# Performance work log

Measured on AMD Instinct MI355X. Metric: run time of the kernel, lower is better.

## Reference

```python
import jax, jax.numpy as jnp
import numpy as np

N_QUBITS = 4
N_LAYERS = 2
DIM = 2 ** N_QUBITS


def _cnot_perm(c, t, n=N_QUBITS):
    # statevector index bit for wire w is at shift (n-1-w)
    idx = np.arange(2 ** n)
    cbit = (idx >> (n - 1 - c)) & 1
    return np.where(cbit == 1, idx ^ (1 << (n - 1 - t)), idx)


def _apply_cnot(state, c, t):
    # state: [B, 2,2,2,2]; CNOT is a basis permutation (its own inverse)
    B = state.shape[0]
    flat = state.reshape(B, DIM)
    return flat[:, _cnot_perm(c, t)].reshape(state.shape)


def _apply_1q(state, U, wire):
    # shared 2x2 gate U on given wire
    st = jnp.moveaxis(state, wire + 1, -1)
    st = jnp.einsum('b...a,ca->b...c', st, U)
    return jnp.moveaxis(st, -1, wire + 1)


def _quantum_circuit(z, weights):
    """AngleEmbedding(RY) + StronglyEntanglingLayers, PauliZ expvals.
    z: [B, n_qubits] angles, weights: [L, n_qubits, 3]. Returns [B, n_qubits]."""
    n = N_QUBITS
    B = z.shape[0]
    state = jnp.zeros((B, DIM), jnp.complex64).at[:, 0].set(1.0)
    state = state.reshape((B,) + (2,) * n)
    # Angle embedding: batched RY(z_w) on each wire
    for w in range(n):
        a = z[:, w] * 0.5
        c, s = jnp.cos(a), jnp.sin(a)
        U = jnp.stack([jnp.stack([c, -s], -1), jnp.stack([s, c], -1)], -2)  # [B,2,2]
        st = jnp.moveaxis(state, w + 1, -1)
        st = jnp.einsum('b...a,bca->b...c', st, U.astype(jnp.complex64))
        state = jnp.moveaxis(st, -1, w + 1)
    # StronglyEntanglingLayers
    for l in range(N_LAYERS):
        for w in range(n):
            phi, theta, omega = weights[l, w, 0], weights[l, w, 1], weights[l, w, 2]
            ct, st_ = jnp.cos(theta * 0.5), jnp.sin(theta * 0.5)
            e_m = jnp.exp(-0.5j * (phi + omega).astype(jnp.complex64))
            e_d = jnp.exp(0.5j * (phi - omega).astype(jnp.complex64))
            U = jnp.stack([
                jnp.stack([e_m * ct, -e_d * st_]),
                jnp.stack([jnp.conj(e_d) * st_, jnp.conj(e_m) * ct]),
            ])  # Rot(phi,theta,omega) = RZ(omega) RY(theta) RZ(phi)
            state = _apply_1q(state, U, w)
        r = (l % (n - 1)) + 1
        for w in range(n):
            state = _apply_cnot(state, w, (w + r) % n)
    probs = state.real ** 2 + state.imag ** 2  # [B,2,2,2,2]
    evs = []
    rest = tuple(range(1, n))
    for w in range(n):
        p = jnp.moveaxis(probs, w + 1, 1)
        evs.append(jnp.sum(p[:, 0], axis=rest) - jnp.sum(p[:, 1], axis=rest))
    return jnp.stack(evs, -1)


def setup_inputs() -> dict:
    key = jax.random.key(0)
    ks = jax.random.split(key, 6)
    B, C, H, W = 16, 256, 128, 128
    return {
        'x': jax.random.normal(ks[0], (B, C, H, W), jnp.float32),
        'enc_w': jax.random.normal(ks[1], (N_QUBITS, C), jnp.float32) / np.sqrt(C),
        'enc_b': jax.random.normal(ks[2], (N_QUBITS,), jnp.float32) * 0.01,
        'qweights': jax.random.uniform(ks[3], (N_LAYERS, N_QUBITS, 3), jnp.float32, 0.0, 2.0 * np.pi),
        'proj_w': jax.random.normal(ks[4], (C, N_QUBITS), jnp.float32) / np.sqrt(N_QUBITS),
        'proj_b': jax.random.normal(ks[5], (C,), jnp.float32) * 0.01,
    }


def reference(x, enc_w, enc_b, qweights, proj_w, proj_b):
    pooled = jnp.mean(x, axis=(2, 3))                      # AdaptiveAvgPool2d(1)+Flatten -> [B,C]
    z = jnp.tanh(pooled @ enc_w.T + enc_b)                 # [B, n_qubits]
    refined = _quantum_circuit(z, qweights)                # [B, n_qubits]
    gates = jax.nn.sigmoid(refined @ proj_w.T + proj_b)    # [B, C]
    return x + x * gates[:, :, None, None]
```

## Files before the change

### kernel.cpp

```cpp
#include <hip/hip_runtime.h>
#include <math.h>

#define NQ 4
#define NL 2
#define DIM 16
#define BATCH 16
#define CH 256
#define HW 16384

typedef float floatx4 __attribute__((ext_vector_type(4)));

__global__ void pool_kernel(const float* __restrict__ x, float* __restrict__ pooled) {
    const int bc = blockIdx.x;
    const floatx4* x4 = (const floatx4*)(x + (size_t)bc * HW);
    const int tid = threadIdx.x;
    float s = 0.f;
#pragma unroll
    for (int k = 0; k < 16; ++k) {
        floatx4 v = x4[tid + k * 256];
        s += v.x + v.y + v.z + v.w;
    }
#pragma unroll
    for (int off = 32; off > 0; off >>= 1) s += __shfl_down(s, off, 64);
    __shared__ float partial[4];
    if ((tid & 63) == 0) partial[tid >> 6] = s;
    __syncthreads();
    if (tid == 0)
        pooled[bc] = (partial[0] + partial[1] + partial[2] + partial[3]) * (1.0f / HW);
}

__global__ void gate_kernel16(const float* __restrict__ pooled,
                              const float* __restrict__ enc_w,
                              const float* __restrict__ enc_b,
                              const float* __restrict__ qw,
                              const float* __restrict__ proj_w,
                              const float* __restrict__ proj_b,
                              float* __restrict__ gates1p) {
    const int b = blockIdx.x;
    const int tid = threadIdx.x;

    __shared__ float sz[NQ];
    __shared__ float sevs[NQ];

    {
        const int q = tid >> 6, lane = tid & 63;
        const float* prow = pooled + b * CH;
        float acc = 0.f;
#pragma unroll
        for (int j = 0; j < 4; ++j) {
            const int c = lane * 4 + j;
            acc += prow[c] * enc_w[q * CH + c];
        }
#pragma unroll
        for (int off = 32; off > 0; off >>= 1) acc += __shfl_down(acc, off, 64);
        if (lane == 0) sz[q] = tanhf(acc + enc_b[q]);
    }
    __syncthreads();

    if (tid == 0) {
        float re[DIM], im[DIM];
#pragma unroll
        for (int i = 0; i < DIM; ++i) { re[i] = 0.f; im[i] = 0.f; }
        re[0] = 1.f;

        for (int w = 0; w < NQ; ++w) {
            const float a = sz[w] * 0.5f;
            const float cc = cosf(a), ss = sinf(a);
            const int m = 1 << (3 - w);
#pragma unroll
            for (int i = 0; i < DIM; ++i) {
                if (i & m) continue;
                const int j = i | m;
                const float r0 = cc * re[i] - ss * re[j];
                const float i0 = cc * im[i] - ss * im[j];
                const float r1 = ss * re[i] + cc * re[j];
                const float i1 = ss * im[i] + cc * im[j];
                re[i] = r0; im[i] = i0; re[j] = r1; im[j] = i1;
            }
        }
        for (int l = 0; l < NL; ++l) {
            for (int w = 0; w < NQ; ++w) {
                const float phi = qw[(l * NQ + w) * 3 + 0];
                const float th  = qw[(l * NQ + w) * 3 + 1];
                const float om  = qw[(l * NQ + w) * 3 + 2];
                const float ct = cosf(0.5f * th), st = sinf(0.5f * th);
                const float am = -0.5f * (phi + om);
                const float ad =  0.5f * (phi - om);
                const float emr = cosf(am), emi = sinf(am);
                const float edr = cosf(ad), edi = sinf(ad);
                const float u00r =  emr * ct, u00i =  emi * ct;
                const float u01r = -edr * st, u01i = -edi * st;
                const float u10r =  edr * st, u10i = -edi * st;
                const float u11r =  emr * ct, u11i = -emi * ct;
                const int m = 1 << (3 - w);
#pragma unroll
                for (int i = 0; i < DIM; ++i) {
                    if (i & m) continue;
                    const int j = i | m;
                    const float ar = re[i], ai = im[i], br = re[j], bi = im[j];
                    re[i] = u00r * ar - u00i * ai + u01r * br - u01i * bi;
                    im[i] = u00r * ai + u00i * ar + u01r * bi + u01i * br;
                    re[j] = u10r * ar - u10i * ai + u11r * br - u11i * bi;
                    im[j] = u10r * ai + u10i * ar + u11r * bi + u11i * br;
                }
            }
            const int r = (l % (NQ - 1)) + 1;
            for (int w = 0; w < NQ; ++w) {
                const int t = (w + r) % NQ;
                const int cm = 1 << (3 - w);
                const int tm = 1 << (3 - t);
#pragma unroll
                for (int i = 0; i < DIM; ++i) {
                    if ((i & cm) && !(i & tm)) {
                        const int j = i | tm;
                        float tr = re[i]; re[i] = re[j]; re[j] = tr;
                        float ti = im[i]; im[i] = im[j]; im[j] = ti;
                    }
                }
            }
        }
        float p[DIM];
#pragma unroll
        for (int i = 0; i < DIM; ++i) p[i] = re[i] * re[i] + im[i] * im[i];
        for (int w = 0; w < NQ; ++w) {
            const int m = 1 << (3 - w);
            float ev = 0.f;
#pragma unroll
            for (int i = 0; i < DIM; ++i) ev += (i & m) ? -p[i] : p[i];
            sevs[w] = ev;
        }
    }
    __syncthreads();

    {
        const int c = tid;
        const float acc = sevs[0] * proj_w[c * NQ + 0] + sevs[1] * proj_w[c * NQ + 1] +
                          sevs[2] * proj_w[c * NQ + 2] + sevs[3] * proj_w[c * NQ + 3] +
                          proj_b[c];
        gates1p[b * CH + c] = 1.f + 1.f / (1.f + expf(-acc));
    }
}

__global__ void scale_kernel(const float* __restrict__ x,
                             const float* __restrict__ gates1p,
                             float* __restrict__ out) {
    const int slice = 4095 - blockIdx.x;
    const int tid = threadIdx.x;
    const floatx4* x4 = (const floatx4*)(x + (size_t)slice * HW);
    floatx4* o4 = (floatx4*)(out + (size_t)slice * HW);
    const float g = gates1p[slice];
    floatx4 v[16];
#pragma unroll
    for (int k = 0; k < 16; ++k) v[k] = x4[tid + k * 256];
#pragma unroll
    for (int k = 0; k < 16; ++k) {
        v[k] *= g;
        __builtin_nontemporal_store(v[k], &o4[tid + k * 256]);
    }
}

extern "C" void kernel_launch(void* const* d_in, const int* in_sizes, int n_in,
                              void* d_out, int out_size, void* d_ws, size_t ws_size,
                              hipStream_t stream) {
    const float* x      = (const float*)d_in[0];
    const float* enc_w  = (const float*)d_in[1];
    const float* enc_b  = (const float*)d_in[2];
    const float* qw     = (const float*)d_in[3];
    const float* proj_w = (const float*)d_in[4];
    const float* proj_b = (const float*)d_in[5];
    float* out = (float*)d_out;

    float* pooled  = (float*)d_ws;
    float* gates1p = pooled + BATCH * CH;

    pool_kernel<<<BATCH * CH, 256, 0, stream>>>(x, pooled);
    gate_kernel16<<<BATCH, 256, 0, stream>>>(pooled, enc_w, enc_b, qw,
                                             proj_w, proj_b, gates1p);
    scale_kernel<<<BATCH * CH, 256, 0, stream>>>(x, gates1p, out);
}
```

Before: 144.9 us.

## Process batch in four chunks so scale pass rereads x from cache

```diff
diff --git a/kernel.cpp b/kernel.cpp
--- a/kernel.cpp
+++ b/kernel.cpp
@@ -7,11 +7,15 @@
 #define BATCH 16
 #define CH 256
 #define HW 16384
+#define CHUNK_B 4
+#define NCHUNK (BATCH / CHUNK_B)
+#define SLICES_PER_CHUNK (CHUNK_B * CH)
 
 typedef float floatx4 __attribute__((ext_vector_type(4)));
 
-__global__ void pool_kernel(const float* __restrict__ x, float* __restrict__ pooled) {
-    const int bc = blockIdx.x;
+__global__ void pool_kernel(const float* __restrict__ x, float* __restrict__ pooled,
+                            int base_bc) {
+    const int bc = base_bc + blockIdx.x;
     const floatx4* x4 = (const floatx4*)(x + (size_t)bc * HW);
     const int tid = threadIdx.x;
     float s = 0.f;
@@ -35,8 +39,9 @@
                               const float* __restrict__ qw,
                               const float* __restrict__ proj_w,
                               const float* __restrict__ proj_b,
-                              float* __restrict__ gates1p) {
-    const int b = blockIdx.x;
+                              float* __restrict__ gates1p,
+                              int base_b) {
+    const int b = base_b + blockIdx.x;
     const int tid = threadIdx.x;
 
     __shared__ float sz[NQ];
@@ -143,8 +148,9 @@
 
 __global__ void scale_kernel(const float* __restrict__ x,
                              const float* __restrict__ gates1p,
-                             float* __restrict__ out) {
-    const int slice = 4095 - blockIdx.x;
+                             float* __restrict__ out,
+                             int base_bc) {
+    const int slice = base_bc + blockIdx.x;
     const int tid = threadIdx.x;
     const floatx4* x4 = (const floatx4*)(x + (size_t)slice * HW);
     floatx4* o4 = (floatx4*)(out + (size_t)slice * HW);
@@ -173,8 +179,12 @@
     float* pooled  = (float*)d_ws;
     float* gates1p = pooled + BATCH * CH;
 
-    pool_kernel<<<BATCH * CH, 256, 0, stream>>>(x, pooled);
-    gate_kernel16<<<BATCH, 256, 0, stream>>>(pooled, enc_w, enc_b, qw,
-                                             proj_w, proj_b, gates1p);
-    scale_kernel<<<BATCH * CH, 256, 0, stream>>>(x, gates1p, out);
+    for (int k = 0; k < NCHUNK; ++k) {
+        const int base_bc = k * SLICES_PER_CHUNK;
+        const int base_b  = k * CHUNK_B;
+        pool_kernel<<<SLICES_PER_CHUNK, 256, 0, stream>>>(x, pooled, base_bc);
+        gate_kernel16<<<CHUNK_B, 256, 0, stream>>>(pooled, enc_w, enc_b, qw,
+                                                   proj_w, proj_b, gates1p, base_b);
+        scale_kernel<<<SLICES_PER_CHUNK, 256, 0, stream>>>(x, gates1p, out, base_bc);
+    }
 }
```

Result: slower. 229.8 us (+58.6%).

## Fuse gate computation into scale kernel, recomputing circuit per channel block

Applied to the files above, without the earlier changes.

```diff
diff --git a/kernel.cpp b/kernel.cpp
--- a/kernel.cpp
+++ b/kernel.cpp
@@ -29,18 +29,31 @@
         pooled[bc] = (partial[0] + partial[1] + partial[2] + partial[3]) * (1.0f / HW);
 }
 
-__global__ void gate_kernel16(const float* __restrict__ pooled,
-                              const float* __restrict__ enc_w,
-                              const float* __restrict__ enc_b,
-                              const float* __restrict__ qw,
-                              const float* __restrict__ proj_w,
-                              const float* __restrict__ proj_b,
-                              float* __restrict__ gates1p) {
-    const int b = blockIdx.x;
+__global__ void scale_gate_kernel(
+    const float* __restrict__ x,
+    const float* __restrict__ enc_w,
+    const float* __restrict__ enc_b,
+    const float* __restrict__ qw,
+    const float* __restrict__ proj_w,
+    const float* __restrict__ proj_b,
+    const float* __restrict__ pooled,
+    float* __restrict__ out)
+{
+    const int slice = 4095 - blockIdx.x;
     const int tid = threadIdx.x;
+    const int b = slice >> 8;
+    const int c = slice & 255;
+
+    const floatx4* x4 = (const floatx4*)(x + (size_t)slice * HW);
+    floatx4* o4 = (floatx4*)(out + (size_t)slice * HW);
+
+    floatx4 v[16];
+#pragma unroll
+    for (int k = 0; k < 16; ++k) v[k] = x4[tid + k * 256];
 
     __shared__ float sz[NQ];
     __shared__ float sevs[NQ];
+    __shared__ float sg;
 
     {
         const int q = tid >> 6, lane = tid & 63;
@@ -48,8 +61,8 @@
         float acc = 0.f;
 #pragma unroll
         for (int j = 0; j < 4; ++j) {
-            const int c = lane * 4 + j;
-            acc += prow[c] * enc_w[q * CH + c];
+            const int ch = lane * 4 + j;
+            acc += prow[ch] * enc_w[q * CH + ch];
         }
 #pragma unroll
         for (int off = 32; off > 0; off >>= 1) acc += __shfl_down(acc, off, 64);
@@ -122,36 +135,22 @@
         float p[DIM];
 #pragma unroll
         for (int i = 0; i < DIM; ++i) p[i] = re[i] * re[i] + im[i] * im[i];
+        float evs[NQ];
         for (int w = 0; w < NQ; ++w) {
             const int m = 1 << (3 - w);
             float ev = 0.f;
 #pragma unroll
             for (int i = 0; i < DIM; ++i) ev += (i & m) ? -p[i] : p[i];
-            sevs[w] = ev;
+            evs[w] = ev;
         }
+        const float acc = evs[0] * proj_w[c * NQ + 0] + evs[1] * proj_w[c * NQ + 1] +
+                          evs[2] * proj_w[c * NQ + 2] + evs[3] * proj_w[c * NQ + 3] +
+                          proj_b[c];
+        sg = 1.f + 1.f / (1.f + expf(-acc));
     }
     __syncthreads();
 
-    {
-        const int c = tid;
-        const float acc = sevs[0] * proj_w[c * NQ + 0] + sevs[1] * proj_w[c * NQ + 1] +
-                          sevs[2] * proj_w[c * NQ + 2] + sevs[3] * proj_w[c * NQ + 3] +
-                          proj_b[c];
-        gates1p[b * CH + c] = 1.f + 1.f / (1.f + expf(-acc));
-    }
-}
-
-__global__ void scale_kernel(const float* __restrict__ x,
-                             const float* __restrict__ gates1p,
-                             float* __restrict__ out) {
-    const int slice = 4095 - blockIdx.x;
-    const int tid = threadIdx.x;
-    const floatx4* x4 = (const floatx4*)(x + (size_t)slice * HW);
-    floatx4* o4 = (floatx4*)(out + (size_t)slice * HW);
-    const float g = gates1p[slice];
-    floatx4 v[16];
-#pragma unroll
-    for (int k = 0; k < 16; ++k) v[k] = x4[tid + k * 256];
+    const float g = sg;
 #pragma unroll
     for (int k = 0; k < 16; ++k) {
         v[k] *= g;
@@ -170,11 +169,9 @@
     const float* proj_b = (const float*)d_in[5];
     float* out = (float*)d_out;
 
-    float* pooled  = (float*)d_ws;
-    float* gates1p = pooled + BATCH * CH;
+    float* pooled = (float*)d_ws;
 
     pool_kernel<<<BATCH * CH, 256, 0, stream>>>(x, pooled);
-    gate_kernel16<<<BATCH, 256, 0, stream>>>(pooled, enc_w, enc_b, qw,
-                                             proj_w, proj_b, gates1p);
-    scale_kernel<<<BATCH * CH, 256, 0, stream>>>(x, gates1p, out);
+    scale_gate_kernel<<<BATCH * CH, 256, 0, stream>>>(x, enc_w, enc_b, qw,
+                                                      proj_w, proj_b, pooled, out);
 }
```

Result: slower. 201.0 us (+38.7%).
